# Performance work log

Measured on AMD Instinct MI355X. Metric: run time of the kernel, lower is better.

The kernel has to match this reference:

```python
import jax, jax.numpy as jnp
import numpy as np

D, H, Wd, V, OUTF = 256, 512, 512, 32, 256


def setup_inputs() -> dict:
    key = jax.random.key(0)
    k1, k2, k3, k4 = jax.random.split(key, 4)
    X = jax.random.normal(k1, (1, D, H, Wd), dtype=jnp.float32)
    W = jax.random.normal(k2, (D, V), dtype=jnp.float32)
    # variance is divided by; keep it bounded away from zero
    variance = jax.random.uniform(k3, (D, V), dtype=jnp.float32, minval=0.5, maxval=1.5)
    weight = jax.random.normal(k4, (D, OUTF), dtype=jnp.float32) * 0.05
    return {"X": X, "W": W, "variance": variance, "weight": weight}


def reference(X, W, variance, weight):
    _, d, h, w = X.shape
    outf = weight.shape[1]
    # torch does reshape(X, (h, w, d)) -> flatten to (h*w, d); plain reshape, faithful
    Xf = jnp.reshape(X, (h * w, d))
    iv = 1.0 / variance          # (d, V)
    iv2 = iv * iv
    # Q[p,i] = sum_d ((x_pd - W_di) / var_di)^2, expanded into 2 GEMMs + bias
    Q = (Xf * Xf) @ iv2 - 2.0 * (Xf @ (W * iv2)) + jnp.sum(W * W * iv2, axis=0)[None, :]
    Q = Q - jnp.min(Q, axis=1, keepdims=True)
    Q = jnp.exp(-0.5 * Q)
    Q = Q / jnp.sum(Q, axis=1, keepdims=True)      # (hw, V) row-stochastic
    s = jnp.sum(Q, axis=0)                          # (V,)
    # Z[:,i] = sum_p Q_pi * (x_p - W[:,i]) / var[:,i] / s_i
    Z = ((Xf.T @ Q) - W * s[None, :]) * iv / s[None, :]   # (d, V)
    # original divides by sum of squares (not its sqrt) -- keep faithful
    Z = Z / jnp.sum(Z * Z, axis=0, keepdims=True)
    Adj = Z.T @ Z                                   # (V, V)
    Zo = jax.nn.relu(Adj @ (Z.T @ weight))          # (V, outf)
    Xn = Q @ Zo                                     # (hw, outf)
    # torch: reshape (h, w, outf) then .view(1, outf, h, w) == plain reshape
    return jnp.reshape(Xn, (1, outf, h, w))
```

## Files before the change

kernel.cpp:

```cpp
#include <hip/hip_runtime.h>

#define D_    256
#define V_    32
#define HW_   (512*512)
#define OUTF_ 256

__global__ __launch_bounds__(256) void k1_q(const float* __restrict__ X,
                                            const float* __restrict__ W,
                                            const float* __restrict__ var,
                                            float* __restrict__ Q,
                                            float* __restrict__ s_out)
{
    __shared__ float As[D_][V_];
    __shared__ float Bs[D_][V_];
    const int tid = threadIdx.x;

    {
        const float* wr = W   + tid * V_;
        const float* vr = var + tid * V_;
        #pragma unroll
        for (int i = 0; i < V_; ++i) {
            float iv = 1.0f / vr[i];
            As[tid][i] = wr[i] * iv;
            Bs[tid][i] = iv;
        }
    }
    __syncthreads();

    const size_t pA = (size_t)blockIdx.x * 512 + tid;
    const size_t pB = pA + 256;
    const float4* xrowA = (const float4*)(X + pA * D_);
    const float4* xrowB = (const float4*)(X + pB * D_);

    float tA[V_], tB[V_];
    #pragma unroll
    for (int i = 0; i < V_; ++i) { tA[i] = 0.f; tB[i] = 0.f; }

    for (int d4 = 0; d4 < D_/4; ++d4) {
        float4 xa = xrowA[d4];
        float4 xb = xrowB[d4];
        float xsa[4] = {xa.x, xa.y, xa.z, xa.w};
        float xsb[4] = {xb.x, xb.y, xb.z, xb.w};
        #pragma unroll
        for (int k = 0; k < 4; ++k) {
            const int d = d4*4 + k;
            const float xA = xsa[k];
            const float xB = xsb[k];
            #pragma unroll
            for (int i = 0; i < V_; ++i) {
                const float bi = Bs[d][i];
                const float ai = As[d][i];
                float eA = fmaf(xA, bi, -ai);
                float eB = fmaf(xB, bi, -ai);
                tA[i] = fmaf(eA, eA, tA[i]);
                tB[i] = fmaf(eB, eB, tB[i]);
            }
        }
    }

    float qA[V_], qB[V_];
    float mnA = 3.4e38f, mnB = 3.4e38f;
    #pragma unroll
    for (int i = 0; i < V_; ++i) { mnA = fminf(mnA, tA[i]); mnB = fminf(mnB, tB[i]); }
    float sumA = 0.f, sumB = 0.f;
    #pragma unroll
    for (int i = 0; i < V_; ++i) {
        qA[i] = __expf(-0.5f * (tA[i] - mnA));  sumA += qA[i];
        qB[i] = __expf(-0.5f * (tB[i] - mnB));  sumB += qB[i];
    }
    const float invA = 1.0f / sumA;
    const float invB = 1.0f / sumB;

    float4* qoutA = (float4*)(Q + pA * V_);
    float4* qoutB = (float4*)(Q + pB * V_);
    #pragma unroll
    for (int j = 0; j < V_/4; ++j) {
        float4 oa, ob;
        oa.x = qA[4*j+0]*invA; oa.y = qA[4*j+1]*invA; oa.z = qA[4*j+2]*invA; oa.w = qA[4*j+3]*invA;
        ob.x = qB[4*j+0]*invB; ob.y = qB[4*j+1]*invB; ob.z = qB[4*j+2]*invB; ob.w = qB[4*j+3]*invB;
        qoutA[j] = oa;
        qoutB[j] = ob;
    }

    __syncthreads();
    float* s_blk = &As[0][0];
    if (tid < V_) s_blk[tid] = 0.f;
    __syncthreads();
    #pragma unroll
    for (int i = 0; i < V_; ++i) {
        atomicAdd(&s_blk[i], qA[i]*invA + qB[i]*invB);
    }
    __syncthreads();
    if (tid < V_) atomicAdd(&s_out[tid], s_blk[tid]);
}

#define K2_PXB   512
#define K2_CHUNK 128

__global__ __launch_bounds__(256) void k2_m(const float* __restrict__ X,
                                            const float* __restrict__ Q,
                                            float* __restrict__ M)
{
    __shared__ __align__(16) float Qs[2][K2_CHUNK][V_];
    const int t = threadIdx.x;
    const size_t p0 = (size_t)blockIdx.x * K2_PXB;

    float acc[V_];
    #pragma unroll
    for (int i = 0; i < V_; ++i) acc[i] = 0.f;

    {
        const float4* src = (const float4*)(Q + p0 * V_);
        float4* dst = (float4*)(&Qs[0][0][0]);
        #pragma unroll
        for (int k = 0; k < 4; ++k) dst[t + 256*k] = src[t + 256*k];
    }

    for (int c = 0; c < K2_PXB/K2_CHUNK; ++c) {
        __syncthreads();
        if (c + 1 < K2_PXB/K2_CHUNK) {
            const float4* src = (const float4*)(Q + (p0 + (size_t)(c+1)*K2_CHUNK) * V_);
            float4* dst = (float4*)(&Qs[(c+1)&1][0][0]);
            #pragma unroll
            for (int k = 0; k < 4; ++k) dst[t + 256*k] = src[t + 256*k];
        }

        const float* xb = X + (p0 + (size_t)c*K2_CHUNK) * D_ + t;
        const float (*qb)[V_] = Qs[c&1];

        #pragma unroll 16
        for (int pp = 0; pp < K2_CHUNK; ++pp) {
            const float x = xb[(size_t)pp * D_];
            const float4* q4 = (const float4*)(&qb[pp][0]);
            #pragma unroll
            for (int j = 0; j < 8; ++j) {
                float4 q = q4[j];
                acc[4*j+0] = fmaf(x, q.x, acc[4*j+0]);
                acc[4*j+1] = fmaf(x, q.y, acc[4*j+1]);
                acc[4*j+2] = fmaf(x, q.z, acc[4*j+2]);
                acc[4*j+3] = fmaf(x, q.w, acc[4*j+3]);
            }
        }
    }

    #pragma unroll
    for (int i = 0; i < V_; ++i) atomicAdd(&M[t*V_ + i], acc[i]);
}

__global__ __launch_bounds__(256) void k3a(const float* __restrict__ M,
                                           const float* __restrict__ s_in,
                                           const float* __restrict__ W,
                                           const float* __restrict__ var,
                                           float* __restrict__ Z,
                                           float* __restrict__ Adj)
{
    __shared__ float Zl[D_][V_];
    __shared__ float ss[V_];
    __shared__ float nrm[V_];
    const int t = threadIdx.x;
    if (t < V_) ss[t] = s_in[t];
    __syncthreads();

    #pragma unroll
    for (int i = 0; i < V_; ++i) {
        float iv = 1.0f / var[t*V_ + i];
        float z = (M[t*V_ + i] - W[t*V_ + i] * ss[i]) * iv / ss[i];
        Zl[t][i] = z;
    }
    __syncthreads();
    if (t < V_) {
        float n = 0.f;
        for (int d = 0; d < D_; ++d) { float z = Zl[d][t]; n = fmaf(z, z, n); }
        nrm[t] = n;
    }
    __syncthreads();
    #pragma unroll
    for (int i = 0; i < V_; ++i) {
        float z = Zl[t][i] / nrm[i];
        Zl[t][i] = z;
        Z[t*V_ + i] = z;
    }
    __syncthreads();
    #pragma unroll
    for (int e = 0; e < 4; ++e) {
        int idx = t*4 + e;
        int i = idx >> 5, j = idx & 31;
        float a = 0.f;
        for (int d = 0; d < D_; ++d) a = fmaf(Zl[d][i], Zl[d][j], a);
        Adj[idx] = a;
    }
}

__global__ __launch_bounds__(256) void k3b(const float* __restrict__ Z,
                                           const float* __restrict__ weight,
                                           const float* __restrict__ Adj,
                                           float* __restrict__ Zo)
{
    __shared__ float T[V_];
    const int t = threadIdx.x;
    const int f = blockIdx.x;
    if (t < V_) T[t] = 0.f;
    __syncthreads();
    const float wt = weight[t*OUTF_ + f];
    const float* zr = Z + t*V_;
    #pragma unroll
    for (int j = 0; j < V_; ++j) atomicAdd(&T[j], zr[j] * wt);
    __syncthreads();
    if (t < V_) {
        float o = 0.f;
        #pragma unroll
        for (int j = 0; j < V_; ++j) o = fmaf(Adj[t*V_ + j], T[j], o);
        Zo[t*OUTF_ + f] = fmaxf(o, 0.f);
    }
}

__global__ __launch_bounds__(256) void k4_out(const float* __restrict__ Q,
                                              const float* __restrict__ Zo,
                                              float* __restrict__ out)
{
    __shared__ __align__(16) float Qt[256][V_];
    const int t  = threadIdx.x;
    const int fq = t & 63;
    const int w  = t >> 6;
    const size_t p0 = (size_t)blockIdx.x * 256;

    float zc[4][V_];
    #pragma unroll
    for (int i = 0; i < V_; ++i) {
        float4 z = ((const float4*)(Zo + i*OUTF_))[fq];
        zc[0][i] = z.x; zc[1][i] = z.y; zc[2][i] = z.z; zc[3][i] = z.w;
    }

    {
        float4* dst = (float4*)(&Qt[0][0]);
        const float4* src = (const float4*)(Q + p0 * V_);
        #pragma unroll
        for (int k = 0; k < 8; ++k) dst[t + 256*k] = src[t + 256*k];
    }
    __syncthreads();

    float4* out4 = (float4*)(out + (p0 + (size_t)w*64) * OUTF_);
    #pragma unroll 2
    for (int pp = 0; pp < 64; ++pp) {
        const int p = w*64 + pp;
        const float4* q4 = (const float4*)(&Qt[p][0]);
        float a0 = 0.f, a1 = 0.f, a2 = 0.f, a3 = 0.f;
        #pragma unroll
        for (int j = 0; j < 8; ++j) {
            float4 q = q4[j];
            a0 = fmaf(q.x, zc[0][4*j+0], a0);
            a1 = fmaf(q.x, zc[1][4*j+0], a1);
            a2 = fmaf(q.x, zc[2][4*j+0], a2);
            a3 = fmaf(q.x, zc[3][4*j+0], a3);
            a0 = fmaf(q.y, zc[0][4*j+1], a0);
            a1 = fmaf(q.y, zc[1][4*j+1], a1);
            a2 = fmaf(q.y, zc[2][4*j+1], a2);
            a3 = fmaf(q.y, zc[3][4*j+1], a3);
            a0 = fmaf(q.z, zc[0][4*j+2], a0);
            a1 = fmaf(q.z, zc[1][4*j+2], a1);
            a2 = fmaf(q.z, zc[2][4*j+2], a2);
            a3 = fmaf(q.z, zc[3][4*j+2], a3);
            a0 = fmaf(q.w, zc[0][4*j+3], a0);
            a1 = fmaf(q.w, zc[1][4*j+3], a1);
            a2 = fmaf(q.w, zc[2][4*j+3], a2);
            a3 = fmaf(q.w, zc[3][4*j+3], a3);
        }
        float4 o; o.x = a0; o.y = a1; o.z = a2; o.w = a3;
        out4[pp*64 + fq] = o;
    }
}

extern "C" void kernel_launch(void* const* d_in, const int* in_sizes, int n_in,
                              void* d_out, int out_size, void* d_ws, size_t ws_size,
                              hipStream_t stream)
{
    const float* X      = (const float*)d_in[0];
    const float* W      = (const float*)d_in[1];
    const float* var    = (const float*)d_in[2];
    const float* weight = (const float*)d_in[3];
    float* out = (float*)d_out;
    float* ws  = (float*)d_ws;

    float* Q   = ws;
    float* s   = Q   + (size_t)HW_ * V_;
    float* M   = s   + V_;
    float* Z   = M   + D_ * V_;
    float* Adj = Z   + D_ * V_;
    float* Zo  = Adj + V_ * V_;

    hipMemsetAsync(s, 0, (V_ + D_*V_) * sizeof(float), stream);

    k1_q <<<HW_/512, 256, 0, stream>>>(X, W, var, Q, s);
    k2_m <<<HW_/512, 256, 0, stream>>>(X, Q, M);
    k3a  <<<1,       256, 0, stream>>>(M, s, W, var, Z, Adj);
    k3b  <<<OUTF_,   256, 0, stream>>>(Z, weight, Adj, Zo);
    k4_out<<<HW_/256, 256, 0, stream>>>(Q, Zo, out);
}
```

Measured before the change: 1.190 ms.

## Fuse Q computation and X^T·Q accumulation into one kernel

```diff
diff --git a/kernel.cpp b/kernel.cpp
--- a/kernel.cpp
+++ b/kernel.cpp
@@ -5,14 +5,20 @@
 #define HW_   (512*512)
 #define OUTF_ 256
 
-__global__ __launch_bounds__(256) void k1_q(const float* __restrict__ X,
-                                            const float* __restrict__ W,
-                                            const float* __restrict__ var,
-                                            float* __restrict__ Q,
-                                            float* __restrict__ s_out)
-{
-    __shared__ float As[D_][V_];
-    __shared__ float Bs[D_][V_];
+#define QS_LD 36
+
+__global__ __launch_bounds__(256) void k12_fused(const float* __restrict__ X,
+                                                 const float* __restrict__ W,
+                                                 const float* __restrict__ var,
+                                                 float* __restrict__ Q,
+                                                 float* __restrict__ s_out,
+                                                 float* __restrict__ M)
+{
+    __shared__ float smem[512 * QS_LD];
+    __shared__ float s_blk[V_];
+    float* As = smem;
+    float* Bs = smem + D_ * V_;
+
     const int tid = threadIdx.x;
 
     {
@@ -21,41 +27,58 @@
         #pragma unroll
         for (int i = 0; i < V_; ++i) {
             float iv = 1.0f / vr[i];
-            As[tid][i] = wr[i] * iv;
-            Bs[tid][i] = iv;
-        }
-    }
-    __syncthreads();
-
-    const size_t pA = (size_t)blockIdx.x * 512 + tid;
+            As[tid * V_ + i] = wr[i] * iv;
+            Bs[tid * V_ + i] = iv;
+        }
+    }
+    if (tid < V_) s_blk[tid] = 0.f;
+    __syncthreads();
+
+    const size_t p0 = (size_t)blockIdx.x * 512;
+    const size_t pA = p0 + tid;
     const size_t pB = pA + 256;
-    const float4* xrowA = (const float4*)(X + pA * D_);
-    const float4* xrowB = (const float4*)(X + pB * D_);
+
+    const float4* xrA = (const float4*)(X + pA * D_);
+    const float4* xrB = (const float4*)(X + pB * D_);
 
     float tA[V_], tB[V_];
     #pragma unroll
     for (int i = 0; i < V_; ++i) { tA[i] = 0.f; tB[i] = 0.f; }
 
-    for (int d4 = 0; d4 < D_/4; ++d4) {
-        float4 xa = xrowA[d4];
-        float4 xb = xrowB[d4];
-        float xsa[4] = {xa.x, xa.y, xa.z, xa.w};
-        float xsb[4] = {xb.x, xb.y, xb.z, xb.w};
+    float4 cA[4], cB[4], nA[4], nB[4];
+    #pragma unroll
+    for (int k = 0; k < 4; ++k) { cA[k] = xrA[k]; cB[k] = xrB[k]; }
+
+    for (int g = 0; g < 16; ++g) {
+        if (g < 15) {
+            #pragma unroll
+            for (int k = 0; k < 4; ++k) {
+                nA[k] = xrA[(g + 1) * 4 + k];
+                nB[k] = xrB[(g + 1) * 4 + k];
+            }
+        }
         #pragma unroll
         for (int k = 0; k < 4; ++k) {
-            const int d = d4*4 + k;
-            const float xA = xsa[k];
-            const float xB = xsb[k];
+            float xsa[4] = {cA[k].x, cA[k].y, cA[k].z, cA[k].w};
+            float xsb[4] = {cB[k].x, cB[k].y, cB[k].z, cB[k].w};
             #pragma unroll
-            for (int i = 0; i < V_; ++i) {
-                const float bi = Bs[d][i];
-                const float ai = As[d][i];
-                float eA = fmaf(xA, bi, -ai);
-                float eB = fmaf(xB, bi, -ai);
-                tA[i] = fmaf(eA, eA, tA[i]);
-                tB[i] = fmaf(eB, eB, tB[i]);
+            for (int e = 0; e < 4; ++e) {
+                const int d = g * 16 + k * 4 + e;
+                const float xA = xsa[e];
+                const float xB = xsb[e];
+                #pragma unroll
+                for (int i = 0; i < V_; ++i) {
+                    const float bi = Bs[d * V_ + i];
+                    const float ai = As[d * V_ + i];
+                    float eA = fmaf(xA, bi, -ai);
+                    float eB = fmaf(xB, bi, -ai);
+                    tA[i] = fmaf(eA, eA, tA[i]);
+                    tB[i] = fmaf(eB, eB, tB[i]);
+                }
             }
         }
+        #pragma unroll
+        for (int k = 0; k < 4; ++k) { cA[k] = nA[k]; cB[k] = nB[k]; }
     }
 
     float qA[V_], qB[V_];
@@ -71,80 +94,74 @@
     const float invA = 1.0f / sumA;
     const float invB = 1.0f / sumB;
 
-    float4* qoutA = (float4*)(Q + pA * V_);
-    float4* qoutB = (float4*)(Q + pB * V_);
-    #pragma unroll
-    for (int j = 0; j < V_/4; ++j) {
-        float4 oa, ob;
-        oa.x = qA[4*j+0]*invA; oa.y = qA[4*j+1]*invA; oa.z = qA[4*j+2]*invA; oa.w = qA[4*j+3]*invA;
-        ob.x = qB[4*j+0]*invB; ob.y = qB[4*j+1]*invB; ob.z = qB[4*j+2]*invB; ob.w = qB[4*j+3]*invB;
-        qoutA[j] = oa;
-        qoutB[j] = ob;
-    }
-
-    __syncthreads();
-    float* s_blk = &As[0][0];
-    if (tid < V_) s_blk[tid] = 0.f;
-    __syncthreads();
-    #pragma unroll
-    for (int i = 0; i < V_; ++i) {
-        atomicAdd(&s_blk[i], qA[i]*invA + qB[i]*invB);
-    }
-    __syncthreads();
+    {
+        float4* qoutA = (float4*)(Q + pA * V_);
+        float4* qoutB = (float4*)(Q + pB * V_);
+        #pragma unroll
+        for (int j = 0; j < V_ / 4; ++j) {
+            float4 oa, ob;
+            oa.x = qA[4*j+0]*invA; oa.y = qA[4*j+1]*invA; oa.z = qA[4*j+2]*invA; oa.w = qA[4*j+3]*invA;
+            ob.x = qB[4*j+0]*invB; ob.y = qB[4*j+1]*invB; ob.z = qB[4*j+2]*invB; ob.w = qB[4*j+3]*invB;
+            qoutA[j] = oa;
+            qoutB[j] = ob;
+        }
+    }
+
+    #pragma unroll
+    for (int i = 0; i < V_; ++i) atomicAdd(&s_blk[i], qA[i]*invA + qB[i]*invB);
+
+    __syncthreads();
+    {
+        float4* ra = (float4*)(smem + (size_t)tid * QS_LD);
+        float4* rb = (float4*)(smem + (size_t)(tid + 256) * QS_LD);
+        #pragma unroll
+        for (int j = 0; j < V_ / 4; ++j) {
+            float4 oa, ob;
+            oa.x = qA[4*j+0]*invA; oa.y = qA[4*j+1]*invA; oa.z = qA[4*j+2]*invA; oa.w = qA[4*j+3]*invA;
+            ob.x = qB[4*j+0]*invB; ob.y = qB[4*j+1]*invB; ob.z = qB[4*j+2]*invB; ob.w = qB[4*j+3]*invB;
+            ra[j] = oa;
+            rb[j] = ob;
+        }
+    }
     if (tid < V_) atomicAdd(&s_out[tid], s_blk[tid]);
-}
-
-#define K2_PXB   512
-#define K2_CHUNK 128
-
-__global__ __launch_bounds__(256) void k2_m(const float* __restrict__ X,
-                                            const float* __restrict__ Q,
-                                            float* __restrict__ M)
-{
-    __shared__ __align__(16) float Qs[2][K2_CHUNK][V_];
-    const int t = threadIdx.x;
-    const size_t p0 = (size_t)blockIdx.x * K2_PXB;
-
-    float acc[V_];
-    #pragma unroll
-    for (int i = 0; i < V_; ++i) acc[i] = 0.f;
-
-    {
-        const float4* src = (const float4*)(Q + p0 * V_);
-        float4* dst = (float4*)(&Qs[0][0][0]);
-        #pragma unroll
-        for (int k = 0; k < 4; ++k) dst[t + 256*k] = src[t + 256*k];
-    }
-
-    for (int c = 0; c < K2_PXB/K2_CHUNK; ++c) {
-        __syncthreads();
-        if (c + 1 < K2_PXB/K2_CHUNK) {
-            const float4* src = (const float4*)(Q + (p0 + (size_t)(c+1)*K2_CHUNK) * V_);
-            float4* dst = (float4*)(&Qs[(c+1)&1][0][0]);
+    __syncthreads();
+
+    {
+        float acc[V_];
+        #pragma unroll
+        for (int i = 0; i < V_; ++i) acc[i] = 0.f;
+
+        const float* xb = X + p0 * D_ + tid;
+        float xc[16], xn[16];
+        #pragma unroll
+        for (int k = 0; k < 16; ++k) xc[k] = xb[(size_t)k * D_];
+
+        for (int g = 0; g < 32; ++g) {
+            if (g < 31) {
+                #pragma unroll
+                for (int k = 0; k < 16; ++k)
+                    xn[k] = xb[(size_t)((g + 1) * 16 + k) * D_];
+            }
             #pragma unroll
-            for (int k = 0; k < 4; ++k) dst[t + 256*k] = src[t + 256*k];
-        }
-
-        const float* xb = X + (p0 + (size_t)c*K2_CHUNK) * D_ + t;
-        const float (*qb)[V_] = Qs[c&1];
-
-        #pragma unroll 16
-        for (int pp = 0; pp < K2_CHUNK; ++pp) {
-            const float x = xb[(size_t)pp * D_];
-            const float4* q4 = (const float4*)(&qb[pp][0]);
+            for (int k = 0; k < 16; ++k) {
+                const float x = xc[k];
+                const float4* q4 = (const float4*)(smem + (size_t)(g * 16 + k) * QS_LD);
+                #pragma unroll
+                for (int j = 0; j < 8; ++j) {
+                    float4 q = q4[j];
+                    acc[4*j+0] = fmaf(x, q.x, acc[4*j+0]);
+                    acc[4*j+1] = fmaf(x, q.y, acc[4*j+1]);
+                    acc[4*j+2] = fmaf(x, q.z, acc[4*j+2]);
+                    acc[4*j+3] = fmaf(x, q.w, acc[4*j+3]);
+                }
+            }
             #pragma unroll
-            for (int j = 0; j < 8; ++j) {
-                float4 q = q4[j];
-                acc[4*j+0] = fmaf(x, q.x, acc[4*j+0]);
-                acc[4*j+1] = fmaf(x, q.y, acc[4*j+1]);
-                acc[4*j+2] = fmaf(x, q.z, acc[4*j+2]);
-                acc[4*j+3] = fmaf(x, q.w, acc[4*j+3]);
-            }
-        }
-    }
-
-    #pragma unroll
-    for (int i = 0; i < V_; ++i) atomicAdd(&M[t*V_ + i], acc[i]);
+            for (int k = 0; k < 16; ++k) xc[k] = xn[k];
+        }
+
+        #pragma unroll
+        for (int i = 0; i < V_; ++i) atomicAdd(&M[tid * V_ + i], acc[i]);
+    }
 }
 
 __global__ __launch_bounds__(256) void k3a(const float* __restrict__ M,
@@ -290,8 +307,7 @@
 
     hipMemsetAsync(s, 0, (V_ + D_*V_) * sizeof(float), stream);
 
-    k1_q <<<HW_/512, 256, 0, stream>>>(X, W, var, Q, s);
-    k2_m <<<HW_/512, 256, 0, stream>>>(X, Q, M);
+    k12_fused<<<HW_/512, 256, 0, stream>>>(X, W, var, Q, s, M);
     k3a  <<<1,       256, 0, stream>>>(M, s, W, var, Z, Adj);
     k3b  <<<OUTF_,   256, 0, stream>>>(Z, weight, Adj, Zo);
     k4_out<<<HW_/256, 256, 0, stream>>>(Q, Zo, out);
```

Result: slower. 1.739 ms (+46.2%).
